# Kernel optimization log

Measured on AMD Instinct MI355X. Metric: run time of the kernel, lower is better.

## Reference

```python
import jax, jax.numpy as jnp
import numpy as np
import math

B, L, D = 2, 2048, 4096
H, KVH = 32, 8
HD = D // H          # 128
REP = H // KVH       # 4
THETA = 500000.0


def _rope_tables(seq_len, head_dim, theta):
    inv_freq = 1.0 / (theta ** (np.arange(0, head_dim, 2, dtype=np.float32) / head_dim))
    t = np.arange(seq_len, dtype=np.float32)
    ang = np.outer(t, inv_freq)  # [L, HD//2]
    return jnp.asarray(np.cos(ang)), jnp.asarray(np.sin(ang))


def apply_rope(x, cos, sin):
    # x: [B, L, h, HD]; pairs (x[...,2i], x[...,2i+1]) form complex numbers
    xr, xi = x[..., 0::2], x[..., 1::2]
    c = cos[None, :, None, :]
    s = sin[None, :, None, :]
    out_r = xr * c - xi * s
    out_i = xr * s + xi * c
    return jnp.stack([out_r, out_i], axis=-1).reshape(x.shape)


def setup_inputs() -> dict:
    key = jax.random.key(0)
    ks = jax.random.split(key, 5)
    scale = 1.0 / math.sqrt(D)
    x = jax.random.normal(ks[0], (B, L, D), dtype=jnp.float32)
    wq = jax.random.normal(ks[1], (D, H * HD), dtype=jnp.float32) * scale
    wk = jax.random.normal(ks[2], (D, KVH * HD), dtype=jnp.float32) * scale
    wv = jax.random.normal(ks[3], (D, KVH * HD), dtype=jnp.float32) * scale
    wo = jax.random.normal(ks[4], (H * HD, D), dtype=jnp.float32) * scale
    freqs_cos, freqs_sin = _rope_tables(L, HD, THETA)
    # causal additive mask [L, start_pos+L] with start_pos=0
    mask = jnp.triu(jnp.full((L, L), -1e9, dtype=jnp.float32), k=1)
    return {"x": x, "wq": wq, "wk": wk, "wv": wv, "wo": wo,
            "freqs_cos": freqs_cos, "freqs_sin": freqs_sin,
            "mask": mask, "start_pos": 0}


def reference(x, wq, wk, wv, wo, freqs_cos, freqs_sin, mask, start_pos):
    b, l, _ = x.shape
    q = jnp.einsum('bld,de->ble', x, wq).reshape(b, l, H, HD)
    k = jnp.einsum('bld,de->ble', x, wk).reshape(b, l, KVH, HD)
    v = jnp.einsum('bld,de->ble', x, wv).reshape(b, l, KVH, HD)
    q = apply_rope(q, freqs_cos, freqs_sin)
    k = apply_rope(k, freqs_cos, freqs_sin)
    # KV-cache append with start_pos=0 and max_seq_len=L: cached keys/values == k, v
    # GQA: repeat_interleave kv heads (repeat_kv)
    k = jnp.repeat(k, REP, axis=2)  # [B, L, H, HD]
    v = jnp.repeat(v, REP, axis=2)
    scores = jnp.einsum('blhd,bmhd->bhlm', q, k) / math.sqrt(HD)
    scores = scores + mask[None, None, :, :]
    probs = jax.nn.softmax(scores.astype(jnp.float32), axis=-1).astype(q.dtype)
    out = jnp.einsum('bhlm,bmhd->blhd', probs, v).reshape(b, l, H * HD)
    return jnp.einsum('ble,ed->bld', out, wo)
```

## Files before the change

kernel.cpp:

```cpp
#include <hip/hip_runtime.h>
#include <hip/hip_bf16.h>
#include <stdint.h>


typedef __attribute__((ext_vector_type(8))) short short8;
typedef __attribute__((ext_vector_type(4))) float floatx4;

__device__ __forceinline__ unsigned short f2bf(float f) {
    union { float f; uint32_t u; } v; v.f = f;
    uint32_t u = v.u;
    return (unsigned short)((u + 0x7fffu + ((u >> 16) & 1u)) >> 16);
}

__device__ __forceinline__ float bf2f(unsigned short h) {
    union { uint32_t u; float f; } v; v.u = (uint32_t)h << 16; return v.f;
}

__device__ __forceinline__ void g2l16(const void* g, void* l) {
    __builtin_amdgcn_global_load_lds(
        (__attribute__((address_space(1))) void*)g,
        (__attribute__((address_space(3))) void*)l,
        16, 0, 0);
}

__global__ __launch_bounds__(256) void cast_x_kernel(const float* __restrict__ X,
                                                     unsigned short* __restrict__ Xb,
                                                     int n4) {
    int i = blockIdx.x * 256 + threadIdx.x;
    if (i < n4) {
        floatx4 v = *(const floatx4*)&X[i * 4];
        unsigned int p0 = (unsigned int)f2bf(v[0]) | ((unsigned int)f2bf(v[1]) << 16);
        unsigned int p1 = (unsigned int)f2bf(v[2]) | ((unsigned int)f2bf(v[3]) << 16);
        uint2 pv; pv.x = p0; pv.y = p1;
        *(uint2*)&Xb[i * 4] = pv;
    }
}

__global__ __launch_bounds__(256) void cast_transpose_kernel(const float* __restrict__ W,
                                                             unsigned short* __restrict__ Wt,
                                                             int N, int rowoff) {
    __shared__ alignas(16) float T[64][65];
    int n0 = blockIdx.x * 64, k0 = blockIdx.y * 64;
    int tid = threadIdx.x;
#pragma unroll
    for (int i = 0; i < 16; ++i) {
        int idx = i * 256 + tid;
        int r = idx >> 6, c = idx & 63;
        T[r][c] = W[(k0 + r) * N + n0 + c];
    }
    __syncthreads();
#pragma unroll
    for (int i = 0; i < 16; ++i) {
        int idx = i * 256 + tid;
        int rn = idx >> 6, ck = idx & 63;
        Wt[(size_t)(rowoff + n0 + rn) * 4096 + k0 + ck] = f2bf(T[ck][rn]);
    }
}

template<bool BF16OUT>
__global__ __launch_bounds__(256) void gemm_bt_kernel(const unsigned short* __restrict__ A,
                                                      const unsigned short* __restrict__ Bt,
                                                      float* __restrict__ Cf,
                                                      unsigned short* __restrict__ Cb,
                                                      int M, int N, int K) {
    __shared__ alignas(16) unsigned short As[128 * 32];
    __shared__ alignas(16) unsigned short Bs[128 * 32];
    const int tid = threadIdx.x;
    const int n0 = blockIdx.x * 128;
    const int m0 = blockIdx.y * 128;
    const int w = tid >> 6, lane = tid & 63, lr = lane & 15, lg = lane >> 4;
    const int wm = (w >> 1) * 64, wn = (w & 1) * 64;

    floatx4 acc[4][4];
#pragma unroll
    for (int i = 0; i < 4; ++i)
#pragma unroll
        for (int j = 0; j < 4; ++j)
            acc[i][j] = (floatx4){0.f, 0.f, 0.f, 0.f};

    const unsigned short* ag = A + (size_t)(m0 + (tid >> 2)) * K + (tid & 3) * 8;
    const unsigned short* bg = Bt + (size_t)(n0 + (tid >> 2)) * K + (tid & 3) * 8;
    const size_t half = (size_t)64 * K;

    for (int k0 = 0; k0 < K; k0 += 32) {
        __syncthreads();
        g2l16(ag + k0,        &As[tid * 8]);
        g2l16(ag + k0 + half, &As[2048 + tid * 8]);
        g2l16(bg + k0,        &Bs[tid * 8]);
        g2l16(bg + k0 + half, &Bs[2048 + tid * 8]);
        __syncthreads();

        short8 a[4], b[4];
#pragma unroll
        for (int mt = 0; mt < 4; ++mt)
            a[mt] = *(const short8*)&As[(wm + mt * 16 + lr) * 32 + lg * 8];
#pragma unroll
        for (int nt = 0; nt < 4; ++nt)
            b[nt] = *(const short8*)&Bs[(wn + nt * 16 + lr) * 32 + lg * 8];
#pragma unroll
        for (int mt = 0; mt < 4; ++mt)
#pragma unroll
            for (int nt = 0; nt < 4; ++nt)
                acc[mt][nt] = __builtin_amdgcn_mfma_f32_16x16x32_bf16(a[mt], b[nt], acc[mt][nt], 0, 0, 0);
    }

#pragma unroll
    for (int mt = 0; mt < 4; ++mt)
#pragma unroll
        for (int nt = 0; nt < 4; ++nt)
#pragma unroll
            for (int r = 0; r < 4; ++r) {
                size_t idx = (size_t)(m0 + wm + mt * 16 + lg * 4 + r) * N + n0 + wn + nt * 16 + lr;
                if (BF16OUT) Cb[idx] = f2bf(acc[mt][nt][r]);
                else         Cf[idx] = acc[mt][nt][r];
            }
}

__global__ __launch_bounds__(256) void rope_qk_kernel(const unsigned short* __restrict__ Cqkv,
                                                      const float* __restrict__ fc,
                                                      const float* __restrict__ fs,
                                                      unsigned short* __restrict__ Qb,
                                                      unsigned short* __restrict__ Kb) {
    int e = blockIdx.x * 256 + threadIdx.x;
    int t = blockIdx.y;
    int b = t >> 11, l = t & 2047;
    if (e < 2048) {
        int h = e >> 6, d2 = e & 63;
        unsigned int xv = *(const unsigned int*)&Cqkv[(size_t)t * 6144 + h * 128 + d2 * 2];
        float xr = bf2f((unsigned short)(xv & 0xffffu));
        float xi = bf2f((unsigned short)(xv >> 16));
        float c = fc[l * 64 + d2], s = fs[l * 64 + d2];
        const float sc = 1.4426950408889634f * 0.08838834764831845f;
        float orr = (xr * c - xi * s) * sc;
        float oii = (xr * s + xi * c) * sc;
        unsigned int pack = (unsigned int)f2bf(orr) | ((unsigned int)f2bf(oii) << 16);
        *(unsigned int*)&Qb[(size_t)((b * 32 + h) * 2048 + l) * 128 + d2 * 2] = pack;
    } else {
        int e2 = e - 2048;
        int kvh = e2 >> 6, d2 = e2 & 63;
        unsigned int xv = *(const unsigned int*)&Cqkv[(size_t)t * 6144 + 4096 + kvh * 128 + d2 * 2];
        float xr = bf2f((unsigned short)(xv & 0xffffu));
        float xi = bf2f((unsigned short)(xv >> 16));
        float c = fc[l * 64 + d2], s = fs[l * 64 + d2];
        float orr = xr * c - xi * s;
        float oii = xr * s + xi * c;
        unsigned int pack = (unsigned int)f2bf(orr) | ((unsigned int)f2bf(oii) << 16);
        *(unsigned int*)&Kb[(size_t)((b * 8 + kvh) * 2048 + l) * 128 + d2 * 2] = pack;
    }
}

__global__ __launch_bounds__(256) void transpose_v_kernel(const unsigned short* __restrict__ Cqkv,
                                                          unsigned short* __restrict__ Vt) {
    __shared__ unsigned short T[64][130];
    int l0 = blockIdx.x * 64;
    int kvh = blockIdx.y;
    int b = blockIdx.z;
    int tid = threadIdx.x;
#pragma unroll
    for (int i = 0; i < 32; ++i) {
        int idx = i * 256 + tid;
        int r = idx >> 7, c = idx & 127;
        T[r][c] = Cqkv[(size_t)(b * 2048 + l0 + r) * 6144 + 5120 + kvh * 128 + c];
    }
    __syncthreads();
#pragma unroll
    for (int i = 0; i < 32; ++i) {
        int idx = i * 256 + tid;
        int d = idx >> 6, lx = idx & 63;
        Vt[((size_t)(b * 8 + kvh) * 128 + d) * 2048 + l0 + lx] = T[lx][d];
    }
}

__global__ __launch_bounds__(256) void attn_kernel(const unsigned short* __restrict__ Qb,
                                                   const unsigned short* __restrict__ Kb,
                                                   const unsigned short* __restrict__ Vt,
                                                   unsigned short* __restrict__ AO) {
    __shared__ alignas(16) unsigned short K_lds[64 * 128];
    __shared__ alignas(16) unsigned short V_lds[128 * 64];
    __shared__ alignas(16) unsigned short P_lds[4][16 * 64];

    const int tid = threadIdx.x;
    const int qt = (int)gridDim.x - 1 - (int)blockIdx.x;
    const int h = blockIdx.y, b = blockIdx.z;
    const int kvh = h >> 2;
    const int q0 = qt * 64;
    const int w = tid >> 6, lane = tid & 63, lr = lane & 15, lg = lane >> 4;
    const int sw = lr & 7;

    const unsigned short* Q  = Qb + (size_t)((b * 32 + h) * 2048) * 128;
    const unsigned short* Kp = Kb + (size_t)((b * 8 + kvh) * 2048) * 128;
    const unsigned short* Vp = Vt + (size_t)((b * 8 + kvh) * 128) * 2048;

    short8 qa[4];
#pragma unroll
    for (int f = 0; f < 4; ++f)
        qa[f] = *(const short8*)&Q[(q0 + w * 16 + lr) * 128 + f * 32 + lg * 8];

    short8 ones;
#pragma unroll
    for (int j = 0; j < 8; ++j) ones[j] = (short)0x3F80;

    float m_i[4], l_i[4];
    floatx4 o[8];
#pragma unroll
    for (int r = 0; r < 4; ++r) { m_i[r] = -1e30f; l_i[r] = 0.f; }
#pragma unroll
    for (int dt = 0; dt < 8; ++dt) o[dt] = (floatx4){0.f, 0.f, 0.f, 0.f};

    for (int it = 0; it <= qt; ++it) {
        const int k0 = it * 64;
        __syncthreads();
#pragma unroll
        for (int i = 0; i < 4; ++i) {
            int c = i * 256 + tid;
            int krow = c >> 4, kcl = (c & 15) ^ (krow & 7);
            g2l16(&Kp[(size_t)(k0 + krow) * 128 + kcl * 8], &K_lds[c * 8]);
            int vrow = c >> 3, vcl = (c & 7) ^ (vrow & 7);
            g2l16(&Vp[(size_t)vrow * 2048 + k0 + vcl * 8], &V_lds[c * 8]);
        }
        __syncthreads();

        floatx4 s[4];
#pragma unroll
        for (int nt = 0; nt < 4; ++nt) s[nt] = (floatx4){0.f, 0.f, 0.f, 0.f};
#pragma unroll
        for (int nt = 0; nt < 4; ++nt)
#pragma unroll
            for (int f = 0; f < 4; ++f) {
                int cp = (f * 4 + lg) ^ sw;
                short8 kb = *(const short8*)&K_lds[(nt * 16 + lr) * 128 + cp * 8];
                s[nt] = __builtin_amdgcn_mfma_f32_16x16x32_bf16(qa[f], kb, s[nt], 0, 0, 0);
            }

        if (it == qt) {
#pragma unroll
            for (int nt = 0; nt < 4; ++nt)
#pragma unroll
                for (int r = 0; r < 4; ++r)
                    if (nt * 16 + lr > w * 16 + lg * 4 + r) s[nt][r] = -1e30f;
        }

        float mx[4];
#pragma unroll
        for (int r = 0; r < 4; ++r)
            mx[r] = fmaxf(fmaxf(s[0][r], s[1][r]), fmaxf(s[2][r], s[3][r]));
#pragma unroll
        for (int off = 1; off < 16; off <<= 1)
#pragma unroll
            for (int r = 0; r < 4; ++r)
                mx[r] = fmaxf(mx[r], __shfl_xor(mx[r], off, 64));

        float al[4], p[4][4];
#pragma unroll
        for (int r = 0; r < 4; ++r) {
            float mn = fmaxf(m_i[r], mx[r]);
            al[r] = __builtin_amdgcn_exp2f(m_i[r] - mn);
            m_i[r] = mn;
        }
#pragma unroll
        for (int nt = 0; nt < 4; ++nt)
#pragma unroll
            for (int r = 0; r < 4; ++r)
                p[nt][r] = __builtin_amdgcn_exp2f(s[nt][r] - m_i[r]);

#pragma unroll
        for (int nt = 0; nt < 4; ++nt)
#pragma unroll
            for (int r = 0; r < 4; ++r) {
                int col = nt * 16 + lr, row = lg * 4 + r;
                int cp = (col >> 3) ^ (row & 7);
                P_lds[w][row * 64 + cp * 8 + (col & 7)] = f2bf(p[nt][r]);
            }
        asm volatile("s_waitcnt lgkmcnt(0)" ::: "memory");

        short8 pa0 = *(const short8*)&P_lds[w][lr * 64 + ((0 * 4 + lg) ^ sw) * 8];
        short8 pa1 = *(const short8*)&P_lds[w][lr * 64 + ((1 * 4 + lg) ^ sw) * 8];

        floatx4 t = (floatx4){0.f, 0.f, 0.f, 0.f};
        t = __builtin_amdgcn_mfma_f32_16x16x32_bf16(pa0, ones, t, 0, 0, 0);
        t = __builtin_amdgcn_mfma_f32_16x16x32_bf16(pa1, ones, t, 0, 0, 0);

#pragma unroll
        for (int r = 0; r < 4; ++r) l_i[r] = l_i[r] * al[r] + t[r];
#pragma unroll
        for (int dt = 0; dt < 8; ++dt)
#pragma unroll
            for (int r = 0; r < 4; ++r) o[dt][r] *= al[r];

#pragma unroll
        for (int dt = 0; dt < 8; ++dt) {
            int cp = (0 * 4 + lg) ^ sw;
            short8 vb = *(const short8*)&V_lds[(dt * 16 + lr) * 64 + cp * 8];
            o[dt] = __builtin_amdgcn_mfma_f32_16x16x32_bf16(pa0, vb, o[dt], 0, 0, 0);
        }
#pragma unroll
        for (int dt = 0; dt < 8; ++dt) {
            int cp = (1 * 4 + lg) ^ sw;
            short8 vb = *(const short8*)&V_lds[(dt * 16 + lr) * 64 + cp * 8];
            o[dt] = __builtin_amdgcn_mfma_f32_16x16x32_bf16(pa1, vb, o[dt], 0, 0, 0);
        }
    }

#pragma unroll
    for (int dt = 0; dt < 8; ++dt)
#pragma unroll
        for (int r = 0; r < 4; ++r) {
            int q = q0 + w * 16 + lg * 4 + r;
            AO[(size_t)(b * 2048 + q) * 4096 + h * 128 + dt * 16 + lr] = f2bf(o[dt][r] / l_i[r]);
        }
}

extern "C" void kernel_launch(void* const* d_in, const int* in_sizes, int n_in,
                              void* d_out, int out_size, void* d_ws, size_t ws_size,
                              hipStream_t stream) {
    const float* x  = (const float*)d_in[0];
    const float* wq = (const float*)d_in[1];
    const float* wk = (const float*)d_in[2];
    const float* wv = (const float*)d_in[3];
    const float* wo = (const float*)d_in[4];
    const float* fc = (const float*)d_in[5];
    const float* fs = (const float*)d_in[6];
    float* out = (float*)d_out;

    char* ws = (char*)d_ws;
    unsigned short* wqkvt = (unsigned short*)(ws);
    unsigned short* qb    = (unsigned short*)(ws);
    unsigned short* kb    = (unsigned short*)(ws + 33554432);
    unsigned short* vt    = (unsigned short*)(ws + 41943040);
    unsigned short* xb    = (unsigned short*)(ws + 50331648);
    unsigned short* ao    = xb;
    unsigned short* wot   = (unsigned short*)(ws + 83886080);
    unsigned short* cqkv  = (unsigned short*)d_out;

    cast_x_kernel<<<16384, 256, 0, stream>>>(x, xb, 4194304);
    cast_transpose_kernel<<<dim3(64, 64), 256, 0, stream>>>(wq, wqkvt, 4096, 0);
    cast_transpose_kernel<<<dim3(16, 64), 256, 0, stream>>>(wk, wqkvt, 1024, 4096);
    cast_transpose_kernel<<<dim3(16, 64), 256, 0, stream>>>(wv, wqkvt, 1024, 5120);
    cast_transpose_kernel<<<dim3(64, 64), 256, 0, stream>>>(wo, wot, 4096, 0);

    gemm_bt_kernel<true><<<dim3(48, 32), 256, 0, stream>>>(xb, wqkvt, nullptr, cqkv, 4096, 6144, 4096);

    rope_qk_kernel<<<dim3(10, 4096), 256, 0, stream>>>(cqkv, fc, fs, qb, kb);
    transpose_v_kernel<<<dim3(32, 8, 2), 256, 0, stream>>>(cqkv, vt);

    attn_kernel<<<dim3(32, 32, 2), 256, 0, stream>>>(qb, kb, vt, ao);

    gemm_bt_kernel<false><<<dim3(32, 32), 256, 0, stream>>>(ao, wot, out, nullptr, 4096, 4096, 4096);
}
```

Measured before the change: 1.008 ms.

## Enlarge attention query tile to 128 rows and double-buffer K/V loads

The attention kernel now processes 128 query rows per block, with each wave handling two 16-row subtiles, so every K/V tile loaded into LDS serves twice as many queries. K/V loads are double-buffered: the next tile is prefetched while the current one is computed, which removes one barrier per iteration. Waves skip key tiles that lie entirely above their causal diagonal. The cost is higher register and LDS pressure (about 80KB LDS per block), fewer blocks in the grid, and idle waves during the skipped causal tiles.

```diff
diff --git a/kernel.cpp b/kernel.cpp
--- a/kernel.cpp
+++ b/kernel.cpp
@@ -171,143 +171,179 @@
     }
 }
 
-__global__ __launch_bounds__(256) void attn_kernel(const unsigned short* __restrict__ Qb,
-                                                   const unsigned short* __restrict__ Kb,
-                                                   const unsigned short* __restrict__ Vt,
-                                                   unsigned short* __restrict__ AO) {
-    __shared__ alignas(16) unsigned short K_lds[64 * 128];
-    __shared__ alignas(16) unsigned short V_lds[128 * 64];
-    __shared__ alignas(16) unsigned short P_lds[4][16 * 64];
+__global__ __launch_bounds__(256, 2) void attn_kernel(const unsigned short* __restrict__ Qb,
+                                                      const unsigned short* __restrict__ Kb,
+                                                      const unsigned short* __restrict__ Vt,
+                                                      unsigned short* __restrict__ AO) {
+    __shared__ alignas(16) unsigned short K_lds[2][64 * 128];
+    __shared__ alignas(16) unsigned short V_lds[2][128 * 64];
+    __shared__ alignas(16) unsigned short P_lds[4][32 * 64];
 
     const int tid = threadIdx.x;
     const int qt = (int)gridDim.x - 1 - (int)blockIdx.x;
     const int h = blockIdx.y, b = blockIdx.z;
     const int kvh = h >> 2;
-    const int q0 = qt * 64;
+    const int q0 = qt * 128;
     const int w = tid >> 6, lane = tid & 63, lr = lane & 15, lg = lane >> 4;
     const int sw = lr & 7;
+    const int wrow0 = q0 + w * 32;
+    const int wmax  = wrow0 + 31;
 
     const unsigned short* Q  = Qb + (size_t)((b * 32 + h) * 2048) * 128;
     const unsigned short* Kp = Kb + (size_t)((b * 8 + kvh) * 2048) * 128;
     const unsigned short* Vp = Vt + (size_t)((b * 8 + kvh) * 128) * 2048;
 
-    short8 qa[4];
-#pragma unroll
-    for (int f = 0; f < 4; ++f)
-        qa[f] = *(const short8*)&Q[(q0 + w * 16 + lr) * 128 + f * 32 + lg * 8];
+    short8 qa[2][4];
+#pragma unroll
+    for (int st = 0; st < 2; ++st)
+#pragma unroll
+        for (int f = 0; f < 4; ++f)
+            qa[st][f] = *(const short8*)&Q[(wrow0 + st * 16 + lr) * 128 + f * 32 + lg * 8];
 
     short8 ones;
 #pragma unroll
     for (int j = 0; j < 8; ++j) ones[j] = (short)0x3F80;
 
-    float m_i[4], l_i[4];
-    floatx4 o[8];
-#pragma unroll
-    for (int r = 0; r < 4; ++r) { m_i[r] = -1e30f; l_i[r] = 0.f; }
-#pragma unroll
-    for (int dt = 0; dt < 8; ++dt) o[dt] = (floatx4){0.f, 0.f, 0.f, 0.f};
-
-    for (int it = 0; it <= qt; ++it) {
+    float m_i[2][4], l_i[2][4];
+    floatx4 o[2][8];
+#pragma unroll
+    for (int st = 0; st < 2; ++st) {
+#pragma unroll
+        for (int r = 0; r < 4; ++r) { m_i[st][r] = -1e30f; l_i[st][r] = 0.f; }
+#pragma unroll
+        for (int dt = 0; dt < 8; ++dt) o[st][dt] = (floatx4){0.f, 0.f, 0.f, 0.f};
+    }
+
+    const int nIter = 2 * qt + 2;
+
+#define STAGE(it_, bufsel_)                                                        \
+    do {                                                                           \
+        const int k0s = (it_) * 64;                                                \
+        _Pragma("unroll")                                                          \
+        for (int i = 0; i < 4; ++i) {                                              \
+            int c = i * 256 + tid;                                                 \
+            int krow = c >> 4, kcl = (c & 15) ^ (krow & 7);                        \
+            g2l16(&Kp[(size_t)(k0s + krow) * 128 + kcl * 8], &K_lds[bufsel_][c * 8]); \
+            int vrow = c >> 3, vcl = (c & 7) ^ (vrow & 7);                         \
+            g2l16(&Vp[(size_t)vrow * 2048 + k0s + vcl * 8], &V_lds[bufsel_][c * 8]); \
+        }                                                                          \
+    } while (0)
+
+    STAGE(0, 0);
+
+    for (int it = 0; it < nIter; ++it) {
         const int k0 = it * 64;
+        const int bsel = it & 1;
         __syncthreads();
-#pragma unroll
-        for (int i = 0; i < 4; ++i) {
-            int c = i * 256 + tid;
-            int krow = c >> 4, kcl = (c & 15) ^ (krow & 7);
-            g2l16(&Kp[(size_t)(k0 + krow) * 128 + kcl * 8], &K_lds[c * 8]);
-            int vrow = c >> 3, vcl = (c & 7) ^ (vrow & 7);
-            g2l16(&Vp[(size_t)vrow * 2048 + k0 + vcl * 8], &V_lds[c * 8]);
-        }
-        __syncthreads();
-
-        floatx4 s[4];
-#pragma unroll
-        for (int nt = 0; nt < 4; ++nt) s[nt] = (floatx4){0.f, 0.f, 0.f, 0.f};
+        if (it + 1 < nIter) STAGE(it + 1, bsel ^ 1);
+
+        if (k0 > wmax) continue;
+
+        floatx4 s[2][4];
+#pragma unroll
+        for (int st = 0; st < 2; ++st)
+#pragma unroll
+            for (int nt = 0; nt < 4; ++nt) s[st][nt] = (floatx4){0.f, 0.f, 0.f, 0.f};
 #pragma unroll
         for (int nt = 0; nt < 4; ++nt)
 #pragma unroll
             for (int f = 0; f < 4; ++f) {
                 int cp = (f * 4 + lg) ^ sw;
-                short8 kb = *(const short8*)&K_lds[(nt * 16 + lr) * 128 + cp * 8];
-                s[nt] = __builtin_amdgcn_mfma_f32_16x16x32_bf16(qa[f], kb, s[nt], 0, 0, 0);
-            }
-
-        if (it == qt) {
+                short8 kbf = *(const short8*)&K_lds[bsel][(nt * 16 + lr) * 128 + cp * 8];
+                s[0][nt] = __builtin_amdgcn_mfma_f32_16x16x32_bf16(qa[0][f], kbf, s[0][nt], 0, 0, 0);
+                s[1][nt] = __builtin_amdgcn_mfma_f32_16x16x32_bf16(qa[1][f], kbf, s[1][nt], 0, 0, 0);
+            }
+
+        if (k0 + 63 > wrow0) {
+#pragma unroll
+            for (int st = 0; st < 2; ++st)
+#pragma unroll
+                for (int nt = 0; nt < 4; ++nt)
+#pragma unroll
+                    for (int r = 0; r < 4; ++r)
+                        if (k0 + nt * 16 + lr > wrow0 + st * 16 + lg * 4 + r)
+                            s[st][nt][r] = -1e30f;
+        }
+
+        float mx[2][4], al[2][4];
+#pragma unroll
+        for (int st = 0; st < 2; ++st)
+#pragma unroll
+            for (int r = 0; r < 4; ++r)
+                mx[st][r] = fmaxf(fmaxf(s[st][0][r], s[st][1][r]), fmaxf(s[st][2][r], s[st][3][r]));
+#pragma unroll
+        for (int off = 1; off < 16; off <<= 1)
+#pragma unroll
+            for (int st = 0; st < 2; ++st)
+#pragma unroll
+                for (int r = 0; r < 4; ++r)
+                    mx[st][r] = fmaxf(mx[st][r], __shfl_xor(mx[st][r], off, 64));
+
+#pragma unroll
+        for (int st = 0; st < 2; ++st)
+#pragma unroll
+            for (int r = 0; r < 4; ++r) {
+                float mn = fmaxf(m_i[st][r], mx[st][r]);
+                al[st][r] = __builtin_amdgcn_exp2f(m_i[st][r] - mn);
+                m_i[st][r] = mn;
+            }
+
+#pragma unroll
+        for (int st = 0; st < 2; ++st)
 #pragma unroll
             for (int nt = 0; nt < 4; ++nt)
 #pragma unroll
-                for (int r = 0; r < 4; ++r)
-                    if (nt * 16 + lr > w * 16 + lg * 4 + r) s[nt][r] = -1e30f;
+                for (int r = 0; r < 4; ++r) {
+                    float pv = __builtin_amdgcn_exp2f(s[st][nt][r] - m_i[st][r]);
+                    int col = nt * 16 + lr, row = st * 16 + lg * 4 + r;
+                    int cp = (col >> 3) ^ (row & 7);
+                    P_lds[w][row * 64 + cp * 8 + (col & 7)] = f2bf(pv);
+                }
+        asm volatile("s_waitcnt lgkmcnt(0)" ::: "memory");
+
+        short8 pa[2][2];
+#pragma unroll
+        for (int st = 0; st < 2; ++st)
+#pragma unroll
+            for (int kk = 0; kk < 2; ++kk)
+                pa[st][kk] = *(const short8*)&P_lds[w][(st * 16 + lr) * 64 + ((kk * 4 + lg) ^ sw) * 8];
+
+#pragma unroll
+        for (int st = 0; st < 2; ++st) {
+            floatx4 t = (floatx4){0.f, 0.f, 0.f, 0.f};
+            t = __builtin_amdgcn_mfma_f32_16x16x32_bf16(pa[st][0], ones, t, 0, 0, 0);
+            t = __builtin_amdgcn_mfma_f32_16x16x32_bf16(pa[st][1], ones, t, 0, 0, 0);
+#pragma unroll
+            for (int r = 0; r < 4; ++r) l_i[st][r] = l_i[st][r] * al[st][r] + t[r];
+#pragma unroll
+            for (int dt = 0; dt < 8; ++dt)
+#pragma unroll
+                for (int r = 0; r < 4; ++r) o[st][dt][r] *= al[st][r];
         }
 
-        float mx[4];
-#pragma unroll
-        for (int r = 0; r < 4; ++r)
-            mx[r] = fmaxf(fmaxf(s[0][r], s[1][r]), fmaxf(s[2][r], s[3][r]));
-#pragma unroll
-        for (int off = 1; off < 16; off <<= 1)
-#pragma unroll
-            for (int r = 0; r < 4; ++r)
-                mx[r] = fmaxf(mx[r], __shfl_xor(mx[r], off, 64));
-
-        float al[4], p[4][4];
-#pragma unroll
-        for (int r = 0; r < 4; ++r) {
-            float mn = fmaxf(m_i[r], mx[r]);
-            al[r] = __builtin_amdgcn_exp2f(m_i[r] - mn);
-            m_i[r] = mn;
+#pragma unroll
+        for (int kk = 0; kk < 2; ++kk) {
+            int cp = (kk * 4 + lg) ^ sw;
+#pragma unroll
+            for (int dt = 0; dt < 8; ++dt) {
+                short8 vb = *(const short8*)&V_lds[bsel][(dt * 16 + lr) * 64 + cp * 8];
+                o[0][dt] = __builtin_amdgcn_mfma_f32_16x16x32_bf16(pa[0][kk], vb, o[0][dt], 0, 0, 0);
+                o[1][dt] = __builtin_amdgcn_mfma_f32_16x16x32_bf16(pa[1][kk], vb, o[1][dt], 0, 0, 0);
+            }
         }
-#pragma unroll
-        for (int nt = 0; nt < 4; ++nt)
-#pragma unroll
-            for (int r = 0; r < 4; ++r)
-                p[nt][r] = __builtin_amdgcn_exp2f(s[nt][r] - m_i[r]);
-
-#pragma unroll
-        for (int nt = 0; nt < 4; ++nt)
+    }
+#undef STAGE
+
+#pragma unroll
+    for (int st = 0; st < 2; ++st)
+#pragma unroll
+        for (int dt = 0; dt < 8; ++dt)
 #pragma unroll
             for (int r = 0; r < 4; ++r) {
-                int col = nt * 16 + lr, row = lg * 4 + r;
-                int cp = (col >> 3) ^ (row & 7);
-                P_lds[w][row * 64 + cp * 8 + (col & 7)] = f2bf(p[nt][r]);
-            }
-        asm volatile("s_waitcnt lgkmcnt(0)" ::: "memory");
-
-        short8 pa0 = *(const short8*)&P_lds[w][lr * 64 + ((0 * 4 + lg) ^ sw) * 8];
-        short8 pa1 = *(const short8*)&P_lds[w][lr * 64 + ((1 * 4 + lg) ^ sw) * 8];
-
-        floatx4 t = (floatx4){0.f, 0.f, 0.f, 0.f};
-        t = __builtin_amdgcn_mfma_f32_16x16x32_bf16(pa0, ones, t, 0, 0, 0);
-        t = __builtin_amdgcn_mfma_f32_16x16x32_bf16(pa1, ones, t, 0, 0, 0);
-
-#pragma unroll
-        for (int r = 0; r < 4; ++r) l_i[r] = l_i[r] * al[r] + t[r];
-#pragma unroll
-        for (int dt = 0; dt < 8; ++dt)
-#pragma unroll
-            for (int r = 0; r < 4; ++r) o[dt][r] *= al[r];
-
-#pragma unroll
-        for (int dt = 0; dt < 8; ++dt) {
-            int cp = (0 * 4 + lg) ^ sw;
-            short8 vb = *(const short8*)&V_lds[(dt * 16 + lr) * 64 + cp * 8];
-            o[dt] = __builtin_amdgcn_mfma_f32_16x16x32_bf16(pa0, vb, o[dt], 0, 0, 0);
-        }
-#pragma unroll
-        for (int dt = 0; dt < 8; ++dt) {
-            int cp = (1 * 4 + lg) ^ sw;
-            short8 vb = *(const short8*)&V_lds[(dt * 16 + lr) * 64 + cp * 8];
-            o[dt] = __builtin_amdgcn_mfma_f32_16x16x32_bf16(pa1, vb, o[dt], 0, 0, 0);
-        }
-    }
-
-#pragma unroll
-    for (int dt = 0; dt < 8; ++dt)
-#pragma unroll
-        for (int r = 0; r < 4; ++r) {
-            int q = q0 + w * 16 + lg * 4 + r;
-            AO[(size_t)(b * 2048 + q) * 4096 + h * 128 + dt * 16 + lr] = f2bf(o[dt][r] / l_i[r]);
-        }
+                int q = wrow0 + st * 16 + lg * 4 + r;
+                AO[(size_t)(b * 2048 + q) * 4096 + h * 128 + dt * 16 + lr] =
+                    f2bf(o[st][dt][r] / l_i[st][r]);
+            }
 }
 
 extern "C" void kernel_launch(void* const* d_in, const int* in_sizes, int n_in,
@@ -343,7 +379,7 @@
     rope_qk_kernel<<<dim3(10, 4096), 256, 0, stream>>>(cqkv, fc, fs, qb, kb);
     transpose_v_kernel<<<dim3(32, 8, 2), 256, 0, stream>>>(cqkv, vt);
 
-    attn_kernel<<<dim3(32, 32, 2), 256, 0, stream>>>(qb, kb, vt, ao);
+    attn_kernel<<<dim3(16, 32, 2), 256, 0, stream>>>(qb, kb, vt, ao);
 
     gemm_bt_kernel<false><<<dim3(32, 32), 256, 0, stream>>>(ao, wot, out, nullptr, 4096, 4096, 4096);
 }
```

After: 953.4 us. 5.4% less time.
